# Kernel tuning notes

Hardware: AMD Instinct MI355X
Metric: run time of the kernel (lower is better)

The kernel has to match this reference:

```python
import jax, jax.numpy as jnp
import numpy as np

NUM_EMBEDDINGS = 512
EMBEDDING_DIM = 64
COMMITMENT_COST = 0.25


def setup_inputs() -> dict:
    key = jax.random.key(0)
    k1, k2, k3 = jax.random.split(key, 3)
    inputs = jax.random.normal(k1, (32, 64, 64, 64), dtype=jnp.float32)  # NCHW, C=embedding_dim
    labels = jax.random.randint(k2, (32,), 0, 12, dtype=jnp.int64 if jax.config.jax_enable_x64 else jnp.int32)
    # embedding initialized uniform(-1/K, 1/K) as in the torch module
    embedding = jax.random.uniform(k3, (NUM_EMBEDDINGS, EMBEDDING_DIM), dtype=jnp.float32,
                                   minval=-1.0 / NUM_EMBEDDINGS, maxval=1.0 / NUM_EMBEDDINGS)
    return {"inputs": inputs, "labels": labels, "embedding": embedding}


def reference(inputs, labels, embedding):
    # inputs: [B, C, H, W] with C == EMBEDDING_DIM; labels unused (matches original forward)
    x = jnp.transpose(inputs, (0, 2, 3, 1))            # [B, H, W, C]
    input_shape = x.shape
    flat = x.reshape(-1, EMBEDDING_DIM)                # [N, D]

    distances = (jnp.sum(flat * flat, axis=1, keepdims=True)
                 + jnp.sum(embedding * embedding, axis=1)
                 - 2.0 * jnp.matmul(flat, embedding.T))
    encoding_indices = jnp.argmin(distances, axis=1)   # [N]
    encodings = jax.nn.one_hot(encoding_indices, NUM_EMBEDDINGS, dtype=inputs.dtype)  # [N, K]

    # gather is the same math as encodings @ embedding, without the dense matmul
    quantized = embedding[encoding_indices].reshape(input_shape)  # [B, H, W, C]

    e_latent_loss = jnp.mean((jax.lax.stop_gradient(quantized) - x) ** 2)
    q_latent_loss = jnp.mean((quantized - jax.lax.stop_gradient(x)) ** 2)
    loss = q_latent_loss + COMMITMENT_COST * e_latent_loss

    # straight-through estimator
    quantized_st = x + jax.lax.stop_gradient(quantized - x)

    avg_probs = jnp.mean(encodings, axis=0)
    perplexity = jnp.exp(-jnp.sum(avg_probs * jnp.log(avg_probs + 1e-10)))

    return (loss, jnp.transpose(quantized_st, (0, 3, 1, 2)), perplexity, encodings)
```

## Files before the change

kernel.cpp:

```cpp
#include <hip/hip_runtime.h>


#define OFF_Q    1
#define OFF_PERP 8388609
#define OFF_ENC  8388610

typedef float accf4 __attribute__((ext_vector_type(4)));
typedef short bfrag8 __attribute__((ext_vector_type(8)));

__device__ __forceinline__ unsigned short f2bf(float f) {
    union { float f; unsigned u; } v; v.f = f;
    unsigned r = v.u + 0x7FFFu + ((v.u >> 16) & 1u);
    return (unsigned short)(r >> 16);
}

__device__ __forceinline__ void lds_barrier() {
    asm volatile("s_waitcnt lgkmcnt(0)" ::: "memory");
    __builtin_amdgcn_s_barrier();
    asm volatile("" ::: "memory");
}

__global__ __launch_bounds__(512) void vq_prep(const float* __restrict__ emb,
                                               float* __restrict__ Bk,
                                               unsigned* __restrict__ counts) {
    int k = threadIdx.x;
    const float4* e4 = reinterpret_cast<const float4*>(emb) + k * 16;
    float s = 0.f;
    #pragma unroll
    for (int i = 0; i < 16; ++i) {
        float4 v = e4[i];
        s += v.x * v.x + v.y * v.y + v.z * v.z + v.w * v.w;
    }
    Bk[k] = s;
    counts[k] = 0u;
}

__global__ __launch_bounds__(512, 4) void vq_dist(const float* __restrict__ in,
                                                  const float* __restrict__ emb,
                                                  const float* __restrict__ Bk,
                                                  int* __restrict__ idx,
                                                  float* __restrict__ lossPart,
                                                  float* __restrict__ out) {
    __shared__ __align__(16) unsigned short xB[64 * 72];
    __shared__ float sdw[8][64];
    __shared__ int   skw[8][64];
    __shared__ float lossW[8];

    const int tid  = (int)threadIdx.x;
    const int lane = tid & 63;
    const int v    = __builtin_amdgcn_readfirstlane(tid >> 6);
    const int q    = lane >> 4;
    const int cidx = lane & 15;

    bfrag8 efr[4][2];
    #pragma unroll
    for (int tn = 0; tn < 4; ++tn) {
        #pragma unroll
        for (int ks = 0; ks < 2; ++ks) {
            const float* ep = emb + (size_t)(v * 64 + tn * 16 + cidx) * 64 + ks * 32 + q * 8;
            float4 e0 = *reinterpret_cast<const float4*>(ep);
            float4 e1 = *reinterpret_cast<const float4*>(ep + 4);
            bfrag8 b;
            b[0] = (short)f2bf(e0.x); b[1] = (short)f2bf(e0.y);
            b[2] = (short)f2bf(e0.z); b[3] = (short)f2bf(e0.w);
            b[4] = (short)f2bf(e1.x); b[5] = (short)f2bf(e1.y);
            b[6] = (short)f2bf(e1.z); b[7] = (short)f2bf(e1.w);
            efr[tn][ks] = b;
        }
    }
    float4 Bn[4];
    #pragma unroll
    for (int tn = 0; tn < 4; ++tn)
        Bn[tn] = *reinterpret_cast<const float4*>(&Bk[v * 64 + tn * 16 + q * 4]);
    const int kbaseLane = v * 64 + q * 4;

    float lacc = 0.f;

    #pragma unroll 1
    for (int g = 0; g < 4; ++g) {
        const int gab = (int)blockIdx.x * 4 + g;
        const int bb  = gab >> 6;
        const int hh  = gab & 63;
        const size_t rowBase = (size_t)bb * 262144 + (size_t)hh * 64 + (size_t)lane;

        float xs[8];
        bfrag8 xpk;
        #pragma unroll
        for (int cc = 0; cc < 8; ++cc) {
            const float val = in[rowBase + (size_t)(v * 8 + cc) * 4096];
            xs[cc] = val;
            xpk[cc] = (short)f2bf(val);
        }
        *reinterpret_cast<bfrag8*>(&xB[lane * 72 + v * 8]) = xpk;
        lds_barrier();

        #pragma unroll
        for (int rt = 0; rt < 4; ++rt) {
            const bfrag8 x0 = *reinterpret_cast<const bfrag8*>(&xB[(rt * 16 + cidx) * 72 + q * 8]);
            const bfrag8 x1 = *reinterpret_cast<const bfrag8*>(&xB[(rt * 16 + cidx) * 72 + 32 + q * 8]);
            accf4 acc[4];
            #pragma unroll
            for (int tn = 0; tn < 4; ++tn) {
                acc[tn] = (accf4){0.f, 0.f, 0.f, 0.f};
                acc[tn] = __builtin_amdgcn_mfma_f32_16x16x32_bf16(efr[tn][0], x0, acc[tn], 0, 0, 0);
                acc[tn] = __builtin_amdgcn_mfma_f32_16x16x32_bf16(efr[tn][1], x1, acc[tn], 0, 0, 0);
            }
            float best = 3.4e38f; int bk = kbaseLane;
            #pragma unroll
            for (int tn = 0; tn < 4; ++tn) {
                #pragma unroll
                for (int r = 0; r < 4; ++r) {
                    const float Bj = (r == 0) ? Bn[tn].x : (r == 1) ? Bn[tn].y : (r == 2) ? Bn[tn].z : Bn[tn].w;
                    const float d = Bj - 2.0f * acc[tn][r];
                    if (d < best) { best = d; bk = kbaseLane + tn * 16 + r; }
                }
            }
            #pragma unroll
            for (int s = 16; s <= 32; s <<= 1) {
                const float od = __shfl_xor(best, s);
                const int   ok = __shfl_xor(bk, s);
                if (od < best || (od == best && ok < bk)) { best = od; bk = ok; }
            }
            if (q == 0) {
                sdw[v][rt * 16 + cidx] = best;
                skw[v][rt * 16 + cidx] = bk;
            }
        }
        lds_barrier();

        float fd = sdw[0][lane];
        int   fk = skw[0][lane];
        #pragma unroll
        for (int vv = 1; vv < 8; ++vv) {
            const float dv = sdw[vv][lane];
            const int   kv = skw[vv][lane];
            if (dv < fd) { fd = dv; fk = kv; }
        }
        if (v == 0) idx[gab * 64 + lane] = fk;

        const float* __restrict__ eq = emb + (size_t)fk * 64;
        #pragma unroll
        for (int cc = 0; cc < 8; ++cc) {
            const int c = v * 8 + cc;
            const float qv = eq[c];
            const float dd = qv - xs[cc];
            lacc += dd * dd;
            out[OFF_Q + rowBase + (size_t)c * 4096] = xs[cc] + dd;
        }
    }

    #pragma unroll
    for (int off = 32; off > 0; off >>= 1) lacc += __shfl_down(lacc, off);
    if (lane == 0) lossW[v] = lacc;
    lds_barrier();
    if (tid == 0) {
        float s = 0.f;
        #pragma unroll
        for (int i = 0; i < 8; ++i) s += lossW[i];
        lossPart[blockIdx.x] = s;
    }
}

__global__ __launch_bounds__(256) void vq_enc(const int* __restrict__ idx,
                                              unsigned* __restrict__ counts,
                                              float* __restrict__ out) {
    __shared__ int ki[64];
    const int tid = (int)threadIdx.x;
    if (tid < 64) ki[tid] = idx[(int)blockIdx.x * 64 + tid];
    __syncthreads();
    if (tid < 64) atomicAdd(&counts[ki[tid]], 1u);

    const int rh = tid >> 7;
    const int j2 = tid & 127;
    float2* enc2 = reinterpret_cast<float2*>(out + OFF_ENC + (size_t)blockIdx.x * 32768);

    #pragma unroll 4
    for (int r2 = 0; r2 < 32; ++r2) {
        const int row = r2 * 2 + rh;
        const int k = ki[row];
        #pragma unroll
        for (int half = 0; half < 2; ++half) {
            const int jj = j2 + half * 128;
            float2 val;
            val.x = ((k >> 1) == jj && (k & 1) == 0) ? 1.0f : 0.0f;
            val.y = ((k >> 1) == jj && (k & 1) == 1) ? 1.0f : 0.0f;
            enc2[(size_t)row * 256 + jj] = val;
        }
    }
}

__global__ __launch_bounds__(512) void vq_fin(const unsigned* __restrict__ counts,
                                              const float* __restrict__ lossPart,
                                              float* __restrict__ out) {
    __shared__ float red[512];
    __shared__ float lr[512];
    int k = threadIdx.x;
    float p = (float)counts[k] * (1.0f / 131072.0f);
    red[k] = p * logf(p + 1e-10f);
    lr[k] = lossPart[k];
    __syncthreads();
    for (int s = 256; s > 0; s >>= 1) {
        if (k < s) { red[k] += red[k + s]; lr[k] += lr[k + s]; }
        __syncthreads();
    }
    if (k == 0) {
        out[OFF_PERP] = expf(-red[0]);
        float mf = lr[0] * (1.0f / 8388608.0f);
        out[0] = mf + 0.25f * mf;
    }
}

extern "C" void kernel_launch(void* const* d_in, const int* in_sizes, int n_in,
                              void* d_out, int out_size, void* d_ws, size_t ws_size,
                              hipStream_t stream) {
    const float* in  = (const float*)d_in[0];
    const float* emb = (const float*)d_in[2];
    float* out = (float*)d_out;

    float* Bk        = (float*)d_ws;
    unsigned* counts = (unsigned*)((char*)d_ws + 2048);
    float* lossPart  = (float*)((char*)d_ws + 4096);
    int* idx         = (int*)((char*)d_ws + 8192);

    vq_prep<<<1, 512, 0, stream>>>(emb, Bk, counts);
    vq_dist<<<512, 512, 0, stream>>>(in, emb, Bk, idx, lossPart, out);
    vq_enc<<<2048, 256, 0, stream>>>(idx, counts, out);
    vq_fin<<<1, 512, 0, stream>>>(counts, lossPart, out);
}
```

Baseline: 122.5 us.

## Fuse one-hot encoding writes into distance kernel and use LDS histogram

Moves the one-hot encodings write into the distance kernel, so each block writes the rows for the indices it just computed out of shared memory and no longer reloads them. The separate encoding kernel is replaced by a small histogram kernel that bins counts in LDS before issuing global atomics. This removes one large-grid launch and the global atomic contention on counts. The trade-off is an extra barrier plus 256 KB of output stores per group inside the distance kernel, which may lengthen its critical path.

```diff
diff --git a/kernel.cpp b/kernel.cpp
--- a/kernel.cpp
+++ b/kernel.cpp
@@ -44,6 +44,7 @@
     __shared__ __align__(16) unsigned short xB[64 * 72];
     __shared__ float sdw[8][64];
     __shared__ int   skw[8][64];
+    __shared__ int   fkb[64];
     __shared__ float lossW[8];
 
     const int tid  = (int)threadIdx.x;
@@ -136,7 +137,10 @@
             const int   kv = skw[vv][lane];
             if (dv < fd) { fd = dv; fk = kv; }
         }
-        if (v == 0) idx[gab * 64 + lane] = fk;
+        if (v == 0) {
+            idx[gab * 64 + lane] = fk;
+            fkb[lane] = fk;
+        }
 
         const float* __restrict__ eq = emb + (size_t)fk * 64;
         #pragma unroll
@@ -147,6 +151,22 @@
             lacc += dd * dd;
             out[OFF_Q + rowBase + (size_t)c * 4096] = xs[cc] + dd;
         }
+        lds_barrier();
+
+        {
+            float2* enc2 = reinterpret_cast<float2*>(out + OFF_ENC + (size_t)gab * 32768);
+            #pragma unroll
+            for (int c = 0; c < 32; ++c) {
+                const int p = c * 512 + tid;
+                const int row = p >> 8;
+                const int col2 = p & 255;
+                const int k = fkb[row];
+                float2 val;
+                val.x = ((k >> 1) == col2 && (k & 1) == 0) ? 1.0f : 0.0f;
+                val.y = ((k >> 1) == col2 && (k & 1) == 1) ? 1.0f : 0.0f;
+                enc2[p] = val;
+            }
+        }
     }
 
     #pragma unroll
@@ -161,32 +181,19 @@
     }
 }
 
-__global__ __launch_bounds__(256) void vq_enc(const int* __restrict__ idx,
-                                              unsigned* __restrict__ counts,
-                                              float* __restrict__ out) {
-    __shared__ int ki[64];
+__global__ __launch_bounds__(256) void vq_hist(const int* __restrict__ idx,
+                                               unsigned* __restrict__ counts) {
+    __shared__ unsigned h[512];
     const int tid = (int)threadIdx.x;
-    if (tid < 64) ki[tid] = idx[(int)blockIdx.x * 64 + tid];
+    h[tid] = 0u; h[tid + 256] = 0u;
     __syncthreads();
-    if (tid < 64) atomicAdd(&counts[ki[tid]], 1u);
-
-    const int rh = tid >> 7;
-    const int j2 = tid & 127;
-    float2* enc2 = reinterpret_cast<float2*>(out + OFF_ENC + (size_t)blockIdx.x * 32768);
-
-    #pragma unroll 4
-    for (int r2 = 0; r2 < 32; ++r2) {
-        const int row = r2 * 2 + rh;
-        const int k = ki[row];
-        #pragma unroll
-        for (int half = 0; half < 2; ++half) {
-            const int jj = j2 + half * 128;
-            float2 val;
-            val.x = ((k >> 1) == jj && (k & 1) == 0) ? 1.0f : 0.0f;
-            val.y = ((k >> 1) == jj && (k & 1) == 1) ? 1.0f : 0.0f;
-            enc2[(size_t)row * 256 + jj] = val;
-        }
-    }
+    const int base = (int)blockIdx.x * 2048;
+    #pragma unroll
+    for (int i = 0; i < 8; ++i)
+        atomicAdd(&h[idx[base + i * 256 + tid]], 1u);
+    __syncthreads();
+    atomicAdd(&counts[tid], h[tid]);
+    atomicAdd(&counts[tid + 256], h[tid + 256]);
 }
 
 __global__ __launch_bounds__(512) void vq_fin(const unsigned* __restrict__ counts,
@@ -224,6 +231,6 @@
 
     vq_prep<<<1, 512, 0, stream>>>(emb, Bk, counts);
     vq_dist<<<512, 512, 0, stream>>>(in, emb, Bk, idx, lossPart, out);
-    vq_enc<<<2048, 256, 0, stream>>>(idx, counts, out);
+    vq_hist<<<64, 256, 0, stream>>>(idx, counts);
     vq_fin<<<1, 512, 0, stream>>>(counts, lossPart, out);
 }
```

Result: slower. 129.5 us (+5.7%).

## Move quantized output write into encoding kernel and compute loss from distances

Applied to the files above, without the earlier changes.

The distance kernel no longer gathers codebook rows or writes the quantized output. Instead it accumulates ||x||^2 plus the winning bf16-based distance as the loss term. The encoding kernel now stages the selected codebook rows in LDS and writes the quantized tensor, writing the codebook value directly instead of x + (q - x). This moves the scattered gather and store out of the register-heavy MFMA kernel into the write-bound kernel. In exchange, the loss now comes from bf16 distances, which are less accurate, and the straight-through output may differ from x+(q-x) by rounding.

```diff
diff --git a/kernel.cpp b/kernel.cpp
--- a/kernel.cpp
+++ b/kernel.cpp
@@ -83,12 +83,11 @@
         const int hh  = gab & 63;
         const size_t rowBase = (size_t)bb * 262144 + (size_t)hh * 64 + (size_t)lane;
 
-        float xs[8];
         bfrag8 xpk;
         #pragma unroll
         for (int cc = 0; cc < 8; ++cc) {
             const float val = in[rowBase + (size_t)(v * 8 + cc) * 4096];
-            xs[cc] = val;
+            lacc += val * val;
             xpk[cc] = (short)f2bf(val);
         }
         *reinterpret_cast<bfrag8*>(&xB[lane * 72 + v * 8]) = xpk;
@@ -128,24 +127,17 @@
         }
         lds_barrier();
 
-        float fd = sdw[0][lane];
-        int   fk = skw[0][lane];
-        #pragma unroll
-        for (int vv = 1; vv < 8; ++vv) {
-            const float dv = sdw[vv][lane];
-            const int   kv = skw[vv][lane];
-            if (dv < fd) { fd = dv; fk = kv; }
-        }
-        if (v == 0) idx[gab * 64 + lane] = fk;
-
-        const float* __restrict__ eq = emb + (size_t)fk * 64;
-        #pragma unroll
-        for (int cc = 0; cc < 8; ++cc) {
-            const int c = v * 8 + cc;
-            const float qv = eq[c];
-            const float dd = qv - xs[cc];
-            lacc += dd * dd;
-            out[OFF_Q + rowBase + (size_t)c * 4096] = xs[cc] + dd;
+        if (v == 0) {
+            float fd = sdw[0][lane];
+            int   fk = skw[0][lane];
+            #pragma unroll
+            for (int vv = 1; vv < 8; ++vv) {
+                const float dv = sdw[vv][lane];
+                const int   kv = skw[vv][lane];
+                if (dv < fd) { fd = dv; fk = kv; }
+            }
+            idx[gab * 64 + lane] = fk;
+            lacc += fd;
         }
     }
 
@@ -162,17 +154,43 @@
 }
 
 __global__ __launch_bounds__(256) void vq_enc(const int* __restrict__ idx,
+                                              const float* __restrict__ emb,
                                               unsigned* __restrict__ counts,
                                               float* __restrict__ out) {
     __shared__ int ki[64];
+    __shared__ float eqL[64 * 68];
+
     const int tid = (int)threadIdx.x;
-    if (tid < 64) ki[tid] = idx[(int)blockIdx.x * 64 + tid];
+    const int gab = (int)blockIdx.x;
+    const int bb  = gab >> 6;
+    const int hh  = gab & 63;
+
+    if (tid < 64) ki[tid] = idx[gab * 64 + tid];
     __syncthreads();
     if (tid < 64) atomicAdd(&counts[ki[tid]], 1u);
 
+    {
+        const int row = tid >> 2, seg = tid & 3;
+        const float4* ep = reinterpret_cast<const float4*>(emb + (size_t)ki[row] * 64 + seg * 16);
+        float4* dst = reinterpret_cast<float4*>(&eqL[row * 68 + seg * 16]);
+        #pragma unroll
+        for (int i = 0; i < 4; ++i) dst[i] = ep[i];
+    }
+    __syncthreads();
+
+    {
+        const int w = tid & 63, cq = tid >> 6;
+        const size_t qBase = OFF_Q + (size_t)bb * 262144 + (size_t)hh * 64 + (size_t)w;
+        #pragma unroll
+        for (int cc = 0; cc < 16; ++cc) {
+            const int c = cq * 16 + cc;
+            out[qBase + (size_t)c * 4096] = eqL[w * 68 + c];
+        }
+    }
+
     const int rh = tid >> 7;
     const int j2 = tid & 127;
-    float2* enc2 = reinterpret_cast<float2*>(out + OFF_ENC + (size_t)blockIdx.x * 32768);
+    float2* enc2 = reinterpret_cast<float2*>(out + OFF_ENC + (size_t)gab * 32768);
 
     #pragma unroll 4
     for (int r2 = 0; r2 < 32; ++r2) {
@@ -224,6 +242,6 @@
 
     vq_prep<<<1, 512, 0, stream>>>(emb, Bk, counts);
     vq_dist<<<512, 512, 0, stream>>>(in, emb, Bk, idx, lossPart, out);
-    vq_enc<<<2048, 256, 0, stream>>>(idx, counts, out);
+    vq_enc<<<2048, 256, 0, stream>>>(idx, emb, counts, out);
     vq_fin<<<1, 512, 0, stream>>>(counts, lossPart, out);
 }
```

After: 119.7 us. 1.02x faster.
